# Optimization experiments

Measured on AMD Instinct MI355X. Metric: run time of the kernel, lower is better.

Reference implementation:

```python
import jax, jax.numpy as jnp
import numpy as np

MARGIN = 0.3
EPS = 1e-8


def setup_inputs() -> dict:
    key = jax.random.key(0)
    k1, k2 = jax.random.split(key)
    B, D, NUM_IDS = 8192, 128, 1024
    embeddings = jax.random.normal(k1, (B, D), dtype=jnp.float32)
    labels = jax.random.randint(k2, (B,), 0, NUM_IDS, dtype=jnp.int64)
    return {"embeddings": embeddings, "labels": labels}


def _pairwise_distance(embeddings):
    # dist[i,j] = sqrt(relu(||e_i||^2 - 2 e_i.e_j + ||e_j||^2) + eps)
    dot = embeddings @ embeddings.T                       # [B, B]
    sq = jnp.diagonal(dot)                                # [B]
    d2 = sq[None, :] - 2.0 * dot + sq[:, None]
    return jnp.sqrt(jax.nn.relu(d2) + EPS)


def reference(embeddings, labels):
    B = labels.shape[0]
    dist = _pairwise_distance(embeddings)                 # [B, B]

    same = labels[:, None] == labels[None, :]             # [B, B]
    eye = jnp.eye(B, dtype=bool)
    pos_mask = same & ~eye
    neg_mask = ~same

    neg_inf = jnp.finfo(dist.dtype).min
    pos_inf = jnp.finfo(dist.dtype).max
    hardest_pos = jnp.max(jnp.where(pos_mask, dist, neg_inf), axis=1)  # [B]
    hardest_neg = jnp.min(jnp.where(neg_mask, dist, pos_inf), axis=1)  # [B]

    valid = pos_mask.any(axis=1) & neg_mask.any(axis=1)   # [B]
    per_anchor = jax.nn.relu(hardest_pos - hardest_neg + MARGIN)
    loss_sum = jnp.sum(jnp.where(valid, per_anchor, 0.0))
    n_triplets = jnp.sum(valid)
    return loss_sum / jnp.maximum(n_triplets, 1).astype(loss_sum.dtype)
```

## Files before the change

kernel.cpp:

```cpp
#include <hip/hip_runtime.h>

#define BSZ 8192
#define DIM 128
#define MARGIN 0.3f
#define EPS 1e-8f
#define NJ 16
#define JCHUNK 512
#define NT 32

typedef __bf16 bf16x8 __attribute__((ext_vector_type(8)));
typedef float f32x4 __attribute__((ext_vector_type(4)));

__device__ __forceinline__ unsigned enc_ord(float f) {
    unsigned u = __float_as_uint(f);
    return (u & 0x80000000u) ? ~u : (u | 0x80000000u);
}
__device__ __forceinline__ float dec_ord(unsigned e) {
    unsigned u = (e & 0x80000000u) ? (e & 0x7FFFFFFFu) : ~e;
    return __uint_as_float(u);
}


__global__ __launch_bounds__(256) void k_prep(const float* __restrict__ emb,
                                              __bf16* __restrict__ hi,
                                              float* __restrict__ sq,
                                              unsigned* __restrict__ maxp,
                                              unsigned* __restrict__ minn,
                                              float* __restrict__ sumcnt) {
    int row = blockIdx.x * 4 + (threadIdx.x >> 6);
    int lane = threadIdx.x & 63;
    float2 v = *(const float2*)&emb[(size_t)row * DIM + lane * 2];
    union { __bf16 b[2]; unsigned u; } p;
    p.b[0] = (__bf16)v.x;
    p.b[1] = (__bf16)v.y;
    ((unsigned*)hi)[row * 64 + lane] = p.u;
    float s = v.x * v.x + v.y * v.y;
#pragma unroll
    for (int m = 32; m >= 1; m >>= 1) s += __shfl_xor(s, m);
    if (lane == 0) {
        sq[row] = s;
        maxp[row] = 0u;
        minn[row] = 0xFFFFFFFFu;
    }
    if (blockIdx.x == 0 && threadIdx.x == 0) {
        sumcnt[0] = 0.0f;
        ((unsigned*)sumcnt)[1] = 0u;
    }
}

__global__ __launch_bounds__(256, 4) void k_mfma(const __bf16* __restrict__ hi,
                                                 const int* __restrict__ labels,
                                                 const float* __restrict__ sq,
                                                 unsigned* __restrict__ maxp,
                                                 unsigned* __restrict__ minn) {
    __shared__ char Bst[2][4][1024];
    __shared__ float sqlds[JCHUNK];
    __shared__ int lablds[JCHUNK];

    const int tid = threadIdx.x;
    const int lane = tid & 63;
    const int wave = tid >> 6;
    const int lr = lane & 15;
    const int lq = lane >> 4;
    const int it0 = blockIdx.x * 128 + wave * 32;
    const int it1 = it0 + 16;
    const int j0 = blockIdx.y * JCHUNK;
    const float INF = __uint_as_float(0x7F800000u);

#pragma unroll
    for (int s = 0; s < JCHUNK / 256; ++s) {
        sqlds[s * 256 + tid] = sq[j0 + s * 256 + tid];
        lablds[s * 256 + tid] = labels[j0 + s * 256 + tid];
    }

    bf16x8 a0[4], a1[4];
    const __bf16* ap = hi + (size_t)(it0 + lr) * DIM + lq * 8;
#pragma unroll
    for (int f = 0; f < 4; ++f) {
        a0[f] = *(const bf16x8*)&ap[f * 32];
        a1[f] = *(const bf16x8*)&ap[16 * DIM + f * 32];
        asm volatile("" : "+v"(a0[f]));
        asm volatile("" : "+v"(a1[f]));
    }
    const int4 li0 = *(const int4*)&labels[it0 + lq * 4];
    const int4 li1 = *(const int4*)&labels[it1 + lq * 4];
    const int labi0[4] = {li0.x, li0.y, li0.z, li0.w};
    const int labi1[4] = {li1.x, li1.y, li1.z, li1.w};

    float mp0[4], mp1[4], mn0[4], mn1[4];
#pragma unroll
    for (int r = 0; r < 4; ++r) {
        mp0[r] = -INF; mp1[r] = -INF;
        mn0[r] = INF;  mn1[r] = INF;
    }

    const __bf16* bsrc0 = hi + (size_t)(j0 + lr) * DIM + lq * 8 + wave * 32;
#define STAGE(jt, buf)                                                               \
    __builtin_amdgcn_global_load_lds(                                                \
        (const __attribute__((address_space(1))) void*)(bsrc0 + (size_t)(jt) * 16 * DIM), \
        (__attribute__((address_space(3))) void*)&Bst[buf][wave][0], 16, 0, 0)

    STAGE(0, 0);
    __syncthreads();

#pragma unroll 1
    for (int t = 0; t < NT; ++t) {
        if (t + 1 < NT) STAGE(t + 1, (t + 1) & 1);

        const float sqj = sqlds[t * 16 + lr];
        const int labj = lablds[t * 16 + lr];

        const bf16x8* bp = (const bf16x8*)&Bst[t & 1][0][0];
        f32x4 acc0 = {0, 0, 0, 0}, acc1 = {0, 0, 0, 0};
#pragma unroll
        for (int f = 0; f < 4; ++f) {
            bf16x8 b = bp[f * 64 + lane];
            acc0 = __builtin_amdgcn_mfma_f32_16x16x32_bf16(a0[f], b, acc0, 0, 0, 0);
            acc1 = __builtin_amdgcn_mfma_f32_16x16x32_bf16(a1[f], b, acc1, 0, 0, 0);
        }

#pragma unroll
        for (int r = 0; r < 4; ++r) {
            float k0 = fmaf(-2.0f, acc0[r], sqj);
            float k1 = fmaf(-2.0f, acc1[r], sqj);
            bool s0 = (labj == labi0[r]);
            bool s1 = (labj == labi1[r]);
            mp0[r] = s0 ? fmaxf(mp0[r], k0) : mp0[r];
            mn0[r] = s0 ? mn0[r] : fminf(mn0[r], k0);
            mp1[r] = s1 ? fmaxf(mp1[r], k1) : mp1[r];
            mn1[r] = s1 ? mn1[r] : fminf(mn1[r], k1);
        }

        __syncthreads();
    }
#undef STAGE

#pragma unroll
    for (int m = 1; m < 16; m <<= 1) {
#pragma unroll
        for (int r = 0; r < 4; ++r) {
            mp0[r] = fmaxf(mp0[r], __shfl_xor(mp0[r], m));
            mn0[r] = fminf(mn0[r], __shfl_xor(mn0[r], m));
            mp1[r] = fmaxf(mp1[r], __shfl_xor(mp1[r], m));
            mn1[r] = fminf(mn1[r], __shfl_xor(mn1[r], m));
        }
    }
    if (lr == 0) {
#pragma unroll
        for (int r = 0; r < 4; ++r) {
            atomicMax(&maxp[it0 + lq * 4 + r], enc_ord(mp0[r]));
            atomicMin(&minn[it0 + lq * 4 + r], enc_ord(mn0[r]));
            atomicMax(&maxp[it1 + lq * 4 + r], enc_ord(mp1[r]));
            atomicMin(&minn[it1 + lq * 4 + r], enc_ord(mn1[r]));
        }
    }
}

__global__ __launch_bounds__(256) void k_final(const unsigned* __restrict__ maxp,
                                               const unsigned* __restrict__ minn,
                                               const float* __restrict__ sq,
                                               float* __restrict__ sumcnt) {
    int i = blockIdx.x * 256 + threadIdx.x;
    float mpd = dec_ord(maxp[i]);
    float mnd = dec_ord(minn[i]);
    float sqi = sq[i];
    bool valid = (mpd > -1e30f) && (mnd < 1e30f);
    float hp = sqrtf(fmaxf(sqi + mpd, 0.0f) + EPS);
    float hn = sqrtf(fmaxf(sqi + mnd, 0.0f) + EPS);
    float per = valid ? fmaxf(hp - hn + MARGIN, 0.0f) : 0.0f;
    unsigned cnt = valid ? 1u : 0u;
#pragma unroll
    for (int m = 32; m >= 1; m >>= 1) {
        per += __shfl_xor(per, m);
        cnt += __shfl_xor(cnt, m);
    }
    __shared__ float ssum[4];
    __shared__ unsigned scnt[4];
    int wid = threadIdx.x >> 6;
    if ((threadIdx.x & 63) == 0) { ssum[wid] = per; scnt[wid] = cnt; }
    __syncthreads();
    if (threadIdx.x == 0) {
        float s = ssum[0] + ssum[1] + ssum[2] + ssum[3];
        unsigned c = scnt[0] + scnt[1] + scnt[2] + scnt[3];
        atomicAdd(&sumcnt[0], s);
        atomicAdd((unsigned*)&sumcnt[1], c);
    }
}

__global__ void k_out(const float* __restrict__ sumcnt, float* __restrict__ out) {
    if (threadIdx.x == 0) {
        float s = sumcnt[0];
        unsigned c = ((const unsigned*)sumcnt)[1];
        out[0] = s / (float)(c > 0u ? c : 1u);
    }
}

extern "C" void kernel_launch(void* const* d_in, const int* in_sizes, int n_in,
                              void* d_out, int out_size, void* d_ws, size_t ws_size,
                              hipStream_t stream) {
    const float* emb    = (const float*)d_in[0];
    const int*   labels = (const int*)d_in[1];

    __bf16* hi = (__bf16*)d_ws;
    float*  sq = (float*)(hi + (size_t)BSZ * DIM);
    unsigned* maxp = (unsigned*)(sq + BSZ);
    unsigned* minn = maxp + BSZ;
    float* sumcnt = (float*)(minn + BSZ);
    float* out = (float*)d_out;

    k_prep<<<dim3(BSZ / 4), dim3(256), 0, stream>>>(emb, hi, sq, maxp, minn, sumcnt);
    k_mfma<<<dim3(BSZ / 128, NJ), dim3(256), 0, stream>>>(hi, labels, sq, maxp, minn);
    k_final<<<dim3(BSZ / 256), dim3(256), 0, stream>>>(maxp, minn, sq, sumcnt);
    k_out<<<dim3(1), dim3(64), 0, stream>>>(sumcnt, out);
}
```

Before: 46.62 us.

## Process 32 columns per pipeline step and split j across twice as many blocks

The column chunk per block is halved (512 to 256) so the grid doubles to 64x32 blocks. Each loop iteration now stages and processes two 16-column B tiles, issuing four MFMAs per k-slice instead of two. Iterations and barriers per block drop from 32 to 8. The cost is more atomic min/max writes, double the LDS staging buffer, and more live accumulator registers per thread.

```diff
diff --git a/kernel.cpp b/kernel.cpp
--- a/kernel.cpp
+++ b/kernel.cpp
@@ -4,12 +4,15 @@
 #define DIM 128
 #define MARGIN 0.3f
 #define EPS 1e-8f
-#define NJ 16
-#define JCHUNK 512
-#define NT 32
+#define NJ 32
+#define JCHUNK 256
+#define NPH 8
 
 typedef __bf16 bf16x8 __attribute__((ext_vector_type(8)));
 typedef float f32x4 __attribute__((ext_vector_type(4)));
+
+#define AS1 __attribute__((address_space(1)))
+#define AS3 __attribute__((address_space(3)))
 
 __device__ __forceinline__ unsigned enc_ord(float f) {
     unsigned u = __float_as_uint(f);
@@ -53,7 +56,7 @@
                                                  const float* __restrict__ sq,
                                                  unsigned* __restrict__ maxp,
                                                  unsigned* __restrict__ minn) {
-    __shared__ char Bst[2][4][1024];
+    __shared__ char Bst[2][8][1024];
     __shared__ float sqlds[JCHUNK];
     __shared__ int lablds[JCHUNK];
 
@@ -67,11 +70,8 @@
     const int j0 = blockIdx.y * JCHUNK;
     const float INF = __uint_as_float(0x7F800000u);
 
-#pragma unroll
-    for (int s = 0; s < JCHUNK / 256; ++s) {
-        sqlds[s * 256 + tid] = sq[j0 + s * 256 + tid];
-        lablds[s * 256 + tid] = labels[j0 + s * 256 + tid];
-    }
+    sqlds[tid] = sq[j0 + tid];
+    lablds[tid] = labels[j0 + tid];
 
     bf16x8 a0[4], a1[4];
     const __bf16* ap = hi + (size_t)(it0 + lr) * DIM + lq * 8;
@@ -94,41 +94,62 @@
         mn0[r] = INF;  mn1[r] = INF;
     }
 
-    const __bf16* bsrc0 = hi + (size_t)(j0 + lr) * DIM + lq * 8 + wave * 32;
-#define STAGE(jt, buf)                                                               \
-    __builtin_amdgcn_global_load_lds(                                                \
-        (const __attribute__((address_space(1))) void*)(bsrc0 + (size_t)(jt) * 16 * DIM), \
-        (__attribute__((address_space(3))) void*)&Bst[buf][wave][0], 16, 0, 0)
+    const int m0 = wave * 2, m1 = m0 + 1;
+    const __bf16* bsA = hi + (size_t)(j0 + (m0 >> 2) * 16 + lr) * DIM + (m0 & 3) * 32 + lq * 8;
+    const __bf16* bsB = hi + (size_t)(j0 + (m1 >> 2) * 16 + lr) * DIM + (m1 & 3) * 32 + lq * 8;
+#define STAGE(t, buf)                                                              \
+    do {                                                                           \
+        __builtin_amdgcn_global_load_lds(                                          \
+            (const AS1 void*)(bsA + (size_t)(t) * 32 * DIM),                       \
+            (AS3 void*)&Bst[buf][m0][0], 16, 0, 0);                                \
+        __builtin_amdgcn_global_load_lds(                                          \
+            (const AS1 void*)(bsB + (size_t)(t) * 32 * DIM),                       \
+            (AS3 void*)&Bst[buf][m1][0], 16, 0, 0);                                \
+    } while (0)
 
     STAGE(0, 0);
     __syncthreads();
 
 #pragma unroll 1
-    for (int t = 0; t < NT; ++t) {
-        if (t + 1 < NT) STAGE(t + 1, (t + 1) & 1);
-
-        const float sqj = sqlds[t * 16 + lr];
-        const int labj = lablds[t * 16 + lr];
+    for (int t = 0; t < NPH; ++t) {
+        if (t + 1 < NPH) STAGE(t + 1, (t + 1) & 1);
+
+        const float sqj0 = sqlds[t * 32 + lr];
+        const float sqj1 = sqlds[t * 32 + 16 + lr];
+        const int labj0 = lablds[t * 32 + lr];
+        const int labj1 = lablds[t * 32 + 16 + lr];
 
         const bf16x8* bp = (const bf16x8*)&Bst[t & 1][0][0];
-        f32x4 acc0 = {0, 0, 0, 0}, acc1 = {0, 0, 0, 0};
+        f32x4 acc00 = {0, 0, 0, 0}, acc01 = {0, 0, 0, 0};
+        f32x4 acc10 = {0, 0, 0, 0}, acc11 = {0, 0, 0, 0};
 #pragma unroll
         for (int f = 0; f < 4; ++f) {
-            bf16x8 b = bp[f * 64 + lane];
-            acc0 = __builtin_amdgcn_mfma_f32_16x16x32_bf16(a0[f], b, acc0, 0, 0, 0);
-            acc1 = __builtin_amdgcn_mfma_f32_16x16x32_bf16(a1[f], b, acc1, 0, 0, 0);
+            bf16x8 b0 = bp[f * 64 + lane];
+            bf16x8 b1 = bp[(4 + f) * 64 + lane];
+            acc00 = __builtin_amdgcn_mfma_f32_16x16x32_bf16(a0[f], b0, acc00, 0, 0, 0);
+            acc10 = __builtin_amdgcn_mfma_f32_16x16x32_bf16(a1[f], b0, acc10, 0, 0, 0);
+            acc01 = __builtin_amdgcn_mfma_f32_16x16x32_bf16(a0[f], b1, acc01, 0, 0, 0);
+            acc11 = __builtin_amdgcn_mfma_f32_16x16x32_bf16(a1[f], b1, acc11, 0, 0, 0);
         }
 
 #pragma unroll
         for (int r = 0; r < 4; ++r) {
-            float k0 = fmaf(-2.0f, acc0[r], sqj);
-            float k1 = fmaf(-2.0f, acc1[r], sqj);
-            bool s0 = (labj == labi0[r]);
-            bool s1 = (labj == labi1[r]);
-            mp0[r] = s0 ? fmaxf(mp0[r], k0) : mp0[r];
-            mn0[r] = s0 ? mn0[r] : fminf(mn0[r], k0);
-            mp1[r] = s1 ? fmaxf(mp1[r], k1) : mp1[r];
-            mn1[r] = s1 ? mn1[r] : fminf(mn1[r], k1);
+            float k00 = fmaf(-2.0f, acc00[r], sqj0);
+            float k01 = fmaf(-2.0f, acc01[r], sqj1);
+            float k10 = fmaf(-2.0f, acc10[r], sqj0);
+            float k11 = fmaf(-2.0f, acc11[r], sqj1);
+            bool s00 = (labj0 == labi0[r]);
+            bool s01 = (labj1 == labi0[r]);
+            bool s10 = (labj0 == labi1[r]);
+            bool s11 = (labj1 == labi1[r]);
+            mp0[r] = s00 ? fmaxf(mp0[r], k00) : mp0[r];
+            mn0[r] = s00 ? mn0[r] : fminf(mn0[r], k00);
+            mp0[r] = s01 ? fmaxf(mp0[r], k01) : mp0[r];
+            mn0[r] = s01 ? mn0[r] : fminf(mn0[r], k01);
+            mp1[r] = s10 ? fmaxf(mp1[r], k10) : mp1[r];
+            mn1[r] = s10 ? mn1[r] : fminf(mn1[r], k10);
+            mp1[r] = s11 ? fmaxf(mp1[r], k11) : mp1[r];
+            mn1[r] = s11 ? mn1[r] : fminf(mn1[r], k11);
         }
 
         __syncthreads();
```

After: 49.05 us. 1.05x slower.
